# Performance work log

Hardware: AMD Instinct MI355X
Metric: run time of the kernel (lower is better)

Reference implementation:

```python
import jax, jax.numpy as jnp
import numpy as np

B, CK, CQ, CV, CO, H, W = 4, 256, 256, 256, 64, 24, 24


def setup_inputs() -> dict:
    key = jax.random.key(0)
    ks = jax.random.split(key, 9)
    s = lambda k, shape, fan: jax.random.normal(k, shape, jnp.float32) * (fan ** -0.5)
    return {
        "key": jax.random.normal(ks[0], (B, CK, H, W), jnp.float32),
        "query": jax.random.normal(ks[1], (B, CQ, H, W), jnp.float32),
        "value": jax.random.normal(ks[2], (B, CV, H, W), jnp.float32),
        "Wk": s(ks[3], (CO, CK), CK),   # 1x1 conv weight for key transform
        "bk": jnp.zeros((CO,), jnp.float32),
        "Wq": s(ks[4], (CO, CQ), CQ),   # 1x1 conv weight for query transform
        "bq": jnp.zeros((CO,), jnp.float32),
        "wf": s(ks[5], (CO,), CO),      # channel-flattening 1x1 conv (CO -> 1)
        "bf": jnp.zeros((), jnp.float32),
    }


def reference(key, query, value, Wk, bk, Wq, bq, wf, bf):
    b, _, hq, wq = query.shape
    nk = key.shape[2] * key.shape[3]
    nq = hq * wq
    # 1x1 conv == per-pixel linear; flatten spatial to (B, N, CO)
    k_ = jnp.einsum('bchw,oc->bhwo', key, Wk).reshape(b, nk, -1) + bk
    q_ = jnp.einsum('bchw,oc->bhwo', query, Wq).reshape(b, nq, -1) + bq
    # broadcast add: (B, Nk, 1, CO) + (B, 1, Nq, CO) -> tanh -> reduce channels
    pre = jnp.tanh(k_[:, :, None, :] + q_[:, None, :, :])
    scores = jnp.einsum('bkqc,c->bkq', pre, wf) + bf
    attn = jax.nn.sigmoid(scores)                      # (B, Nk, Nq)
    v_ = value.reshape(b, value.shape[1], nk)          # (B, CV, Nk)
    out = jnp.einsum('bkq,bck->bcq', attn, v_)         # (B, CV, Nq)
    return out.reshape(b, value.shape[1], hq, wq)
```

## Files before the change

kernel.cpp:

```cpp
#include <hip/hip_runtime.h>
#include <hip/hip_bf16.h>

#define BB 4
#define CIN 256
#define CO 64
#define NN 576
#define NKC 18
#define NMT 36
#define NQT 36

typedef __attribute__((ext_vector_type(8))) short short8;
typedef __attribute__((ext_vector_type(4))) float floatx4;

__device__ __forceinline__ unsigned short f2bf(float f) {
    unsigned int u = __float_as_uint(f);
    unsigned int r = (u + 0x7fffu + ((u >> 16) & 1u)) >> 16;
    return (unsigned short)r;
}

__global__ void __launch_bounds__(256) pack_all(
    const float* __restrict__ key, const float* __restrict__ query,
    const float* __restrict__ value,
    const float* __restrict__ Wk, const float* __restrict__ Wq,
    unsigned short* __restrict__ Xp, unsigned short* __restrict__ Wp,
    unsigned short* __restrict__ Vp)
{
    __shared__ float tile[32][33];
    int bid = blockIdx.x;
    int t = threadIdx.x;
    int l = t & 63;
    int w = t >> 6;

    if (bid < 1152) {
        int zb  = bid / 144;
        int r   = bid % 144;
        int n32 = r % 18;
        int kc  = r / 18;
        int z = zb >> 2, b = zb & 3;
        const float* src = z ? query : key;
        int tx = t & 31, ty = t >> 5;
        const float* s = src + ((size_t)b * CIN + (size_t)kc * 32) * NN + n32 * 32;
        #pragma unroll
        for (int j = 0; j < 4; ++j) {
            int cl = ty + j * 8;
            tile[cl][tx] = s[(size_t)cl * NN + tx];
        }
        __syncthreads();
        if (w < 2) {
            int nl = w * 16 + (l & 15);
            int cl = (l >> 4) * 8;
            uint4 o;
            o.x = (unsigned)f2bf(tile[cl + 0][nl]) | ((unsigned)f2bf(tile[cl + 1][nl]) << 16);
            o.y = (unsigned)f2bf(tile[cl + 2][nl]) | ((unsigned)f2bf(tile[cl + 3][nl]) << 16);
            o.z = (unsigned)f2bf(tile[cl + 4][nl]) | ((unsigned)f2bf(tile[cl + 5][nl]) << 16);
            o.w = (unsigned)f2bf(tile[cl + 6][nl]) | ((unsigned)f2bf(tile[cl + 7][nl]) << 16);
            int mt = n32 * 2 + w;
            *(uint4*)(Xp + ((((size_t)z * BB + b) * NMT + mt) * 8 + kc) * 512 + l * 8) = o;
        }
    } else if (bid < 1168) {
        int funit = (bid - 1152) * 4 + w;
        int z  = funit >> 5;
        int nt = (funit >> 3) & 3;
        int kc = funit & 7;
        const float* W = z ? Wq : Wk;
        int o = nt * 16 + (l & 15);
        int c = kc * 32 + (l >> 4) * 8;
        const float4* p = (const float4*)(W + (size_t)o * CIN + c);
        float4 v0 = p[0], v1 = p[1];
        uint4 u;
        u.x = (unsigned)f2bf(v0.x) | ((unsigned)f2bf(v0.y) << 16);
        u.y = (unsigned)f2bf(v0.z) | ((unsigned)f2bf(v0.w) << 16);
        u.z = (unsigned)f2bf(v1.x) | ((unsigned)f2bf(v1.y) << 16);
        u.w = (unsigned)f2bf(v1.z) | ((unsigned)f2bf(v1.w) << 16);
        *(uint4*)(Wp + (((size_t)z * 4 + nt) * 8 + kc) * 512 + l * 8) = u;
    } else {
        int funit = (bid - 1168) * 4 + w;
        int b  = funit / 288;
        int r  = funit % 288;
        int ct = r / 18;
        int kc = r % 18;
        int c = ct * 16 + (l & 15);
        int k = kc * 32 + (l >> 4) * 8;
        const float4* p = (const float4*)(value + ((size_t)b * CIN + c) * NN + k);
        float4 v0 = p[0], v1 = p[1];
        uint4 u;
        u.x = (unsigned)f2bf(v0.x) | ((unsigned)f2bf(v0.y) << 16);
        u.y = (unsigned)f2bf(v0.z) | ((unsigned)f2bf(v0.w) << 16);
        u.z = (unsigned)f2bf(v1.x) | ((unsigned)f2bf(v1.y) << 16);
        u.w = (unsigned)f2bf(v1.z) | ((unsigned)f2bf(v1.w) << 16);
        *(uint4*)(Vp + (((size_t)b * 16 + ct) * NKC + kc) * 512 + l * 8) = u;
    }
}

__global__ void __launch_bounds__(256) proj_exp_mfma(
    const unsigned short* __restrict__ Xp, const unsigned short* __restrict__ Wp,
    const float* __restrict__ bk, const float* __restrict__ bq,
    float* __restrict__ ek, float* __restrict__ eq)
{
    int t = threadIdx.x, l = t & 63, w = t >> 6;
    int gw = blockIdx.x * 4 + w;
    int z  = gw / 144;
    int r  = gw % 144;
    int b  = r / NMT;
    int mt = r % NMT;

    const unsigned short* ab = Xp + ((((size_t)z * BB + b) * NMT + mt) * 8) * 512 + l * 8;
    const unsigned short* wb = Wp + (size_t)z * 32 * 512 + l * 8;

    floatx4 acc[4] = {{0.f,0.f,0.f,0.f},{0.f,0.f,0.f,0.f},
                      {0.f,0.f,0.f,0.f},{0.f,0.f,0.f,0.f}};
    #pragma unroll
    for (int kc = 0; kc < 8; ++kc) {
        short8 a = *(const short8*)(ab + (size_t)kc * 512);
        #pragma unroll
        for (int nt = 0; nt < 4; ++nt) {
            short8 bf8 = *(const short8*)(wb + ((size_t)nt * 8 + kc) * 512);
            acc[nt] = __builtin_amdgcn_mfma_f32_16x16x32_bf16(a, bf8, acc[nt], 0, 0, 0);
        }
    }

    const float* bias = z ? bq : bk;
    float* outp       = z ? eq : ek;
    int n0 = mt * 16;
    #pragma unroll
    for (int nt = 0; nt < 4; ++nt) {
        int o = nt * 16 + (l & 15);
        float bv = bias[o];
        #pragma unroll
        for (int rr = 0; rr < 4; ++rr) {
            int row = (l >> 4) * 4 + rr;
            outp[((size_t)b * NN + n0 + row) * CO + o] = __expf(2.0f * (acc[nt][rr] + bv));
        }
    }
}

__global__ void __launch_bounds__(256, 3) attn_pack_kernel(
    const float* __restrict__ ek, const float* __restrict__ eq,
    const float* __restrict__ wf, const float* __restrict__ bfp,
    unsigned short* __restrict__ Bp)
{
    int b  = blockIdx.z;
    int k0 = blockIdx.y * 32;
    int q0 = blockIdx.x * 64;
    int t  = threadIdx.x;
    int l  = t & 63;
    int w  = __builtin_amdgcn_readfirstlane(t >> 6);

    __shared__ float eqs[64 * 65];
    __shared__ float sc[32 * 65];

    const float4* esrc = (const float4*)(eq + ((size_t)b * NN + q0) * CO);
    #pragma unroll
    for (int i = 0; i < 4; ++i) {
        int f4  = t + i * 256;
        int row = f4 >> 4, c4 = (f4 & 15) * 4;
        float4 v = esrc[f4];
        int a = row * 65 + c4;
        eqs[a + 0] = v.x; eqs[a + 1] = v.y; eqs[a + 2] = v.z; eqs[a + 3] = v.w;
    }

    float4 w2v[16];
    float C = bfp[0];
    const float4* wfp4 = (const float4*)wf;
    #pragma unroll
    for (int i = 0; i < 16; ++i) {
        float4 wv = wfp4[i];
        C += wv.x + wv.y + wv.z + wv.w;
        wv.x *= 2.0f; wv.y *= 2.0f; wv.z *= 2.0f; wv.w *= 2.0f;
        w2v[i] = wv;
    }
    __syncthreads();

    float4 eqv[16];
    #pragma unroll
    for (int i = 0; i < 16; ++i) {
        int a = l * 65 + i * 4;
        eqv[i].x = eqs[a]; eqv[i].y = eqs[a + 1];
        eqv[i].z = eqs[a + 2]; eqv[i].w = eqs[a + 3];
    }

    #pragma unroll 1
    for (int kk = 0; kk < 8; ++kk) {
        int k = k0 + w * 8 + kk;
        const float4* ekr = (const float4*)(ek + ((size_t)b * NN + k) * CO);
        float a0 = 0.f, a1 = 0.f, a2 = 0.f, a3 = 0.f;
        #pragma unroll
        for (int i = 0; i < 16; ++i) {
            float4 k4 = ekr[i];
            float4 e4 = eqv[i];
            float4 w4 = w2v[i];
            a0 = fmaf(w4.x, __builtin_amdgcn_rcpf(fmaf(k4.x, e4.x, 1.0f)), a0);
            a1 = fmaf(w4.y, __builtin_amdgcn_rcpf(fmaf(k4.y, e4.y, 1.0f)), a1);
            a2 = fmaf(w4.z, __builtin_amdgcn_rcpf(fmaf(k4.z, e4.z, 1.0f)), a2);
            a3 = fmaf(w4.w, __builtin_amdgcn_rcpf(fmaf(k4.w, e4.w, 1.0f)), a3);
        }
        float score = C - (a0 + a1) - (a2 + a3);
        float sg = __builtin_amdgcn_rcpf(1.0f + __expf(-score));
        sc[(w * 8 + kk) * 65 + l] = sg;
    }
    __syncthreads();

    int col = w * 16 + (l & 15);
    int row = (l >> 4) * 8;
    uint4 o;
    o.x = (unsigned)f2bf(sc[(row + 0) * 65 + col]) | ((unsigned)f2bf(sc[(row + 1) * 65 + col]) << 16);
    o.y = (unsigned)f2bf(sc[(row + 2) * 65 + col]) | ((unsigned)f2bf(sc[(row + 3) * 65 + col]) << 16);
    o.z = (unsigned)f2bf(sc[(row + 4) * 65 + col]) | ((unsigned)f2bf(sc[(row + 5) * 65 + col]) << 16);
    o.w = (unsigned)f2bf(sc[(row + 6) * 65 + col]) | ((unsigned)f2bf(sc[(row + 7) * 65 + col]) << 16);
    size_t qt = (size_t)blockIdx.x * 4 + w;
    *(uint4*)(Bp + (((size_t)b * NQT + qt) * NKC + blockIdx.y) * 512 + l * 8) = o;
}

__global__ void __launch_bounds__(256) av_mfma_kernel(
    const unsigned short* __restrict__ Vp,
    const unsigned short* __restrict__ Bp,
    float* __restrict__ out)
{
    int b  = blockIdx.z;
    int ct = blockIdx.y;
    int qx = blockIdx.x;
    int t  = threadIdx.x;
    int l  = t & 63;
    int w  = __builtin_amdgcn_readfirstlane(t >> 6);

    floatx4 acc[4] = {{0.f,0.f,0.f,0.f},{0.f,0.f,0.f,0.f},
                      {0.f,0.f,0.f,0.f},{0.f,0.f,0.f,0.f}};

    const unsigned short* abase = Vp + ((size_t)b * 16 + ct) * NKC * 512 + l * 8;
    const unsigned short* bbase = Bp + ((size_t)b * NQT + (size_t)qx * 4) * NKC * 512 + l * 8;

    for (int kc = w; kc < NKC; kc += 4) {
        short8 a = *(const short8*)(abase + (size_t)kc * 512);
        #pragma unroll
        for (int qt = 0; qt < 4; ++qt) {
            short8 bq = *(const short8*)(bbase + ((size_t)qt * NKC + kc) * 512);
            acc[qt] = __builtin_amdgcn_mfma_f32_16x16x32_bf16(a, bq, acc[qt], 0, 0, 0);
        }
    }

    __shared__ float red[4][64][17];
    #pragma unroll
    for (int qt = 0; qt < 4; ++qt)
        #pragma unroll
        for (int r = 0; r < 4; ++r)
            red[w][l][qt * 4 + r] = acc[qt][r];
    __syncthreads();

    int q = qx * 64 + w * 16 + (l & 15);
    #pragma unroll
    for (int r = 0; r < 4; ++r) {
        float s = red[0][l][w * 4 + r] + red[1][l][w * 4 + r]
                + red[2][l][w * 4 + r] + red[3][l][w * 4 + r];
        int c = ct * 16 + (l >> 4) * 4 + r;
        out[((size_t)b * CIN + c) * NN + q] = s;
    }
}

extern "C" void kernel_launch(void* const* d_in, const int* in_sizes, int n_in,
                              void* d_out, int out_size, void* d_ws, size_t ws_size,
                              hipStream_t stream) {
    const float* key   = (const float*)d_in[0];
    const float* query = (const float*)d_in[1];
    const float* value = (const float*)d_in[2];
    const float* Wk    = (const float*)d_in[3];
    const float* bk    = (const float*)d_in[4];
    const float* Wq    = (const float*)d_in[5];
    const float* bq    = (const float*)d_in[6];
    const float* wf    = (const float*)d_in[7];
    const float* bf    = (const float*)d_in[8];
    float* out = (float*)d_out;

    float* ws = (float*)d_ws;
    float* ek = ws;
    float* eq = ek + (size_t)BB * NN * CO;
    unsigned short* Xp = (unsigned short*)(eq + (size_t)BB * NN * CO);
    unsigned short* Wp = Xp + (size_t)2 * BB * NMT * 8 * 512;
    unsigned short* Vp = Wp + (size_t)2 * 4 * 8 * 512;
    unsigned short* Bp = Vp + (size_t)BB * 16 * NKC * 512;

    pack_all<<<1456, 256, 0, stream>>>(key, query, value, Wk, Wq, Xp, Wp, Vp);

    proj_exp_mfma<<<72, 256, 0, stream>>>(Xp, Wp, bk, bq, ek, eq);

    dim3 ga(NN / 64, NN / 32, BB);
    attn_pack_kernel<<<ga, 256, 0, stream>>>(ek, eq, wf, bf, Bp);

    dim3 gm(NN / 64, 16, BB);
    av_mfma_kernel<<<gm, 256, 0, stream>>>(Vp, Bp, out);
}
```

Before: 102.5 us.

## Fuse bf16 packing into projection and AV kernels, drop separate pack pass

Removes the standalone pack_all kernel that converted key/query/value and weights to bf16 MFMA-tiled layouts. The projection now loads a 256x16 fp32 tile into shared memory and converts it to bf16 on the fly, with the weights also converted in registers. The AV kernel reads fp32 values directly and converts them before the MFMA. This saves one kernel launch and a round trip through global memory, at the cost of repeated conversions, less coalesced value loads, and a wider projection grid with one MFMA chain per wave.

```diff
diff --git a/kernel.cpp b/kernel.cpp
--- a/kernel.cpp
+++ b/kernel.cpp
@@ -6,7 +6,6 @@
 #define CO 64
 #define NN 576
 #define NKC 18
-#define NMT 36
 #define NQT 36
 
 typedef __attribute__((ext_vector_type(8))) short short8;
@@ -18,119 +17,63 @@
     return (unsigned short)r;
 }
 
-__global__ void __launch_bounds__(256) pack_all(
+__global__ void __launch_bounds__(256) proj_exp_fused(
     const float* __restrict__ key, const float* __restrict__ query,
-    const float* __restrict__ value,
     const float* __restrict__ Wk, const float* __restrict__ Wq,
-    unsigned short* __restrict__ Xp, unsigned short* __restrict__ Wp,
-    unsigned short* __restrict__ Vp)
-{
-    __shared__ float tile[32][33];
-    int bid = blockIdx.x;
-    int t = threadIdx.x;
-    int l = t & 63;
-    int w = t >> 6;
-
-    if (bid < 1152) {
-        int zb  = bid / 144;
-        int r   = bid % 144;
-        int n32 = r % 18;
-        int kc  = r / 18;
-        int z = zb >> 2, b = zb & 3;
-        const float* src = z ? query : key;
-        int tx = t & 31, ty = t >> 5;
-        const float* s = src + ((size_t)b * CIN + (size_t)kc * 32) * NN + n32 * 32;
-        #pragma unroll
-        for (int j = 0; j < 4; ++j) {
-            int cl = ty + j * 8;
-            tile[cl][tx] = s[(size_t)cl * NN + tx];
-        }
-        __syncthreads();
-        if (w < 2) {
-            int nl = w * 16 + (l & 15);
-            int cl = (l >> 4) * 8;
-            uint4 o;
-            o.x = (unsigned)f2bf(tile[cl + 0][nl]) | ((unsigned)f2bf(tile[cl + 1][nl]) << 16);
-            o.y = (unsigned)f2bf(tile[cl + 2][nl]) | ((unsigned)f2bf(tile[cl + 3][nl]) << 16);
-            o.z = (unsigned)f2bf(tile[cl + 4][nl]) | ((unsigned)f2bf(tile[cl + 5][nl]) << 16);
-            o.w = (unsigned)f2bf(tile[cl + 6][nl]) | ((unsigned)f2bf(tile[cl + 7][nl]) << 16);
-            int mt = n32 * 2 + w;
-            *(uint4*)(Xp + ((((size_t)z * BB + b) * NMT + mt) * 8 + kc) * 512 + l * 8) = o;
-        }
-    } else if (bid < 1168) {
-        int funit = (bid - 1152) * 4 + w;
-        int z  = funit >> 5;
-        int nt = (funit >> 3) & 3;
-        int kc = funit & 7;
-        const float* W = z ? Wq : Wk;
-        int o = nt * 16 + (l & 15);
-        int c = kc * 32 + (l >> 4) * 8;
-        const float4* p = (const float4*)(W + (size_t)o * CIN + c);
-        float4 v0 = p[0], v1 = p[1];
-        uint4 u;
-        u.x = (unsigned)f2bf(v0.x) | ((unsigned)f2bf(v0.y) << 16);
-        u.y = (unsigned)f2bf(v0.z) | ((unsigned)f2bf(v0.w) << 16);
-        u.z = (unsigned)f2bf(v1.x) | ((unsigned)f2bf(v1.y) << 16);
-        u.w = (unsigned)f2bf(v1.z) | ((unsigned)f2bf(v1.w) << 16);
-        *(uint4*)(Wp + (((size_t)z * 4 + nt) * 8 + kc) * 512 + l * 8) = u;
-    } else {
-        int funit = (bid - 1168) * 4 + w;
-        int b  = funit / 288;
-        int r  = funit % 288;
-        int ct = r / 18;
-        int kc = r % 18;
-        int c = ct * 16 + (l & 15);
-        int k = kc * 32 + (l >> 4) * 8;
-        const float4* p = (const float4*)(value + ((size_t)b * CIN + c) * NN + k);
-        float4 v0 = p[0], v1 = p[1];
-        uint4 u;
-        u.x = (unsigned)f2bf(v0.x) | ((unsigned)f2bf(v0.y) << 16);
-        u.y = (unsigned)f2bf(v0.z) | ((unsigned)f2bf(v0.w) << 16);
-        u.z = (unsigned)f2bf(v1.x) | ((unsigned)f2bf(v1.y) << 16);
-        u.w = (unsigned)f2bf(v1.z) | ((unsigned)f2bf(v1.w) << 16);
-        *(uint4*)(Vp + (((size_t)b * 16 + ct) * NKC + kc) * 512 + l * 8) = u;
-    }
-}
-
-__global__ void __launch_bounds__(256) proj_exp_mfma(
-    const unsigned short* __restrict__ Xp, const unsigned short* __restrict__ Wp,
     const float* __restrict__ bk, const float* __restrict__ bq,
     float* __restrict__ ek, float* __restrict__ eq)
 {
+    int nt16 = blockIdx.x;
+    int b    = blockIdx.y;
+    int z    = blockIdx.z;
+    const float* src  = z ? query : key;
+    const float* W    = z ? Wq : Wk;
+    const float* bias = z ? bq : bk;
+    float*       outp = z ? eq : ek;
+
+    __shared__ float tile[256 * 17];
+
     int t = threadIdx.x, l = t & 63, w = t >> 6;
-    int gw = blockIdx.x * 4 + w;
-    int z  = gw / 144;
-    int r  = gw % 144;
-    int b  = r / NMT;
-    int mt = r % NMT;
-
-    const unsigned short* ab = Xp + ((((size_t)z * BB + b) * NMT + mt) * 8) * 512 + l * 8;
-    const unsigned short* wb = Wp + (size_t)z * 32 * 512 + l * 8;
-
-    floatx4 acc[4] = {{0.f,0.f,0.f,0.f},{0.f,0.f,0.f,0.f},
-                      {0.f,0.f,0.f,0.f},{0.f,0.f,0.f,0.f}};
+
+    const float* sbase = src + (size_t)b * CIN * NN + (size_t)nt16 * 16;
+    #pragma unroll
+    for (int i = 0; i < 4; ++i) {
+        int f4  = t + i * 256;
+        int c   = f4 >> 2;
+        int col = (f4 & 3) * 4;
+        float4 v = *(const float4*)(sbase + (size_t)c * NN + col);
+        float* d = &tile[c * 17 + col];
+        d[0] = v.x; d[1] = v.y; d[2] = v.z; d[3] = v.w;
+    }
+    __syncthreads();
+
+    int nt = w;
+    int m  = l & 15;
+    int o  = nt * 16 + (l & 15);
+    floatx4 acc = {0.f, 0.f, 0.f, 0.f};
     #pragma unroll
     for (int kc = 0; kc < 8; ++kc) {
-        short8 a = *(const short8*)(ab + (size_t)kc * 512);
-        #pragma unroll
-        for (int nt = 0; nt < 4; ++nt) {
-            short8 bf8 = *(const short8*)(wb + ((size_t)nt * 8 + kc) * 512);
-            acc[nt] = __builtin_amdgcn_mfma_f32_16x16x32_bf16(a, bf8, acc[nt], 0, 0, 0);
-        }
-    }
-
-    const float* bias = z ? bq : bk;
-    float* outp       = z ? eq : ek;
-    int n0 = mt * 16;
-    #pragma unroll
-    for (int nt = 0; nt < 4; ++nt) {
-        int o = nt * 16 + (l & 15);
-        float bv = bias[o];
-        #pragma unroll
-        for (int rr = 0; rr < 4; ++rr) {
-            int row = (l >> 4) * 4 + rr;
-            outp[((size_t)b * NN + n0 + row) * CO + o] = __expf(2.0f * (acc[nt][rr] + bv));
-        }
+        int cb = kc * 32 + (l >> 4) * 8;
+        short8 a;
+        #pragma unroll
+        for (int j = 0; j < 8; ++j)
+            a[j] = (short)f2bf(tile[(cb + j) * 17 + m]);
+        const float4* p = (const float4*)(W + (size_t)o * CIN + cb);
+        float4 v0 = p[0], v1 = p[1];
+        short8 bfr;
+        bfr[0] = (short)f2bf(v0.x); bfr[1] = (short)f2bf(v0.y);
+        bfr[2] = (short)f2bf(v0.z); bfr[3] = (short)f2bf(v0.w);
+        bfr[4] = (short)f2bf(v1.x); bfr[5] = (short)f2bf(v1.y);
+        bfr[6] = (short)f2bf(v1.z); bfr[7] = (short)f2bf(v1.w);
+        acc = __builtin_amdgcn_mfma_f32_16x16x32_bf16(a, bfr, acc, 0, 0, 0);
+    }
+
+    int n0 = nt16 * 16;
+    float bv = bias[o];
+    #pragma unroll
+    for (int rr = 0; rr < 4; ++rr) {
+        int row = (l >> 4) * 4 + rr;
+        outp[((size_t)b * NN + n0 + row) * CO + o] = __expf(2.0f * (acc[rr] + bv));
     }
 }
 
@@ -212,7 +155,7 @@
 }
 
 __global__ void __launch_bounds__(256) av_mfma_kernel(
-    const unsigned short* __restrict__ Vp,
+    const float* __restrict__ value,
     const unsigned short* __restrict__ Bp,
     float* __restrict__ out)
 {
@@ -226,11 +169,17 @@
     floatx4 acc[4] = {{0.f,0.f,0.f,0.f},{0.f,0.f,0.f,0.f},
                       {0.f,0.f,0.f,0.f},{0.f,0.f,0.f,0.f}};
 
-    const unsigned short* abase = Vp + ((size_t)b * 16 + ct) * NKC * 512 + l * 8;
+    const float* vb = value + ((size_t)b * CIN + ct * 16 + (l & 15)) * NN + (l >> 4) * 8;
     const unsigned short* bbase = Bp + ((size_t)b * NQT + (size_t)qx * 4) * NKC * 512 + l * 8;
 
     for (int kc = w; kc < NKC; kc += 4) {
-        short8 a = *(const short8*)(abase + (size_t)kc * 512);
+        const float4* p = (const float4*)(vb + kc * 32);
+        float4 v0 = p[0], v1 = p[1];
+        short8 a;
+        a[0] = (short)f2bf(v0.x); a[1] = (short)f2bf(v0.y);
+        a[2] = (short)f2bf(v0.z); a[3] = (short)f2bf(v0.w);
+        a[4] = (short)f2bf(v1.x); a[5] = (short)f2bf(v1.y);
+        a[6] = (short)f2bf(v1.z); a[7] = (short)f2bf(v1.w);
         #pragma unroll
         for (int qt = 0; qt < 4; ++qt) {
             short8 bq = *(const short8*)(bbase + ((size_t)qt * NKC + kc) * 512);
@@ -273,18 +222,14 @@
     float* ws = (float*)d_ws;
     float* ek = ws;
     float* eq = ek + (size_t)BB * NN * CO;
-    unsigned short* Xp = (unsigned short*)(eq + (size_t)BB * NN * CO);
-    unsigned short* Wp = Xp + (size_t)2 * BB * NMT * 8 * 512;
-    unsigned short* Vp = Wp + (size_t)2 * 4 * 8 * 512;
-    unsigned short* Bp = Vp + (size_t)BB * 16 * NKC * 512;
-
-    pack_all<<<1456, 256, 0, stream>>>(key, query, value, Wk, Wq, Xp, Wp, Vp);
-
-    proj_exp_mfma<<<72, 256, 0, stream>>>(Xp, Wp, bk, bq, ek, eq);
+    unsigned short* Bp = (unsigned short*)(eq + (size_t)BB * NN * CO);
+
+    dim3 gp(NN / 16, BB, 2);
+    proj_exp_fused<<<gp, 256, 0, stream>>>(key, query, Wk, Wq, bk, bq, ek, eq);
 
     dim3 ga(NN / 64, NN / 32, BB);
     attn_pack_kernel<<<ga, 256, 0, stream>>>(ek, eq, wf, bf, Bp);
 
     dim3 gm(NN / 64, 16, BB);
-    av_mfma_kernel<<<gm, 256, 0, stream>>>(Vp, Bp, out);
-}
+    av_mfma_kernel<<<gm, 256, 0, stream>>>(value, Bp, out);
+}
```

New measurement: 102.9 us. No clear change (+0.5%).
